# Optimization experiments

Measured on AMD Instinct MI355X. Metric: run time of the kernel, lower is better.

Reference implementation:

```python
import jax, jax.numpy as jnp
import numpy as np

B, C, I, E, K, H, W = 8, 16, 1, 256, 3, 256, 256  # batch, channels, input_dim, embedding_dim, kernel, spatial
NUM_CH = 64  # embedding vocabulary (num_channels)
PAD = 1


def setup_inputs() -> dict:
    key = jax.random.key(0)
    k1, k2, k3 = jax.random.split(key, 3)
    x = jax.random.normal(k1, (B, C, I, H, W), dtype=jnp.float32)
    indices = jax.random.randint(k2, (B, C), 0, NUM_CH)
    emb_weight = jax.random.normal(k3, (NUM_CH, I * E * K * K), dtype=jnp.float32) * 0.05
    bias = jnp.zeros((1, E, 1, 1), dtype=jnp.float32)
    return {"x": x, "indices": indices, "emb_weight": emb_weight, "bias": bias}


def reference(x, indices, emb_weight, bias):
    # Gather per-(sample, channel) conv weights: [B, C, I*E*K*K]
    w = emb_weight[indices].astype(x.dtype)
    w = w.reshape(B, C, I, E, K, K)
    # Encoder conv path: permute(0,3,1,2,4,5) -> [B, E, C, I, K, K] -> [B*E, C*I, K, K]
    w = jnp.transpose(w, (0, 3, 1, 2, 4, 5)).reshape(B * E, C * I, K, K)
    # x -> [1, B*C*I, H, W]; grouped conv with groups=B
    xr = x.reshape(1, B * C * I, H, W)
    y = jax.lax.conv_general_dilated(
        xr, w,
        window_strides=(1, 1),
        padding=[(PAD, PAD), (PAD, PAD)],
        feature_group_count=B,
        dimension_numbers=("NCHW", "OIHW", "NCHW"),
    )
    y = y.reshape(B, E, H, W) + bias
    return y
```

## Files before the change

### kernel.cpp

```cpp
#include <hip/hip_runtime.h>
#include <hip/hip_bf16.h>

#define BB 8
#define CC 16
#define EE 256
#define HH 256
#define WW 256
#define EMB_ROW (EE*9)

typedef __attribute__((ext_vector_type(8)))  __bf16 bf16x8;
typedef __attribute__((ext_vector_type(16))) float  f32x16;
typedef __attribute__((ext_vector_type(4)))  float  f32x4;

#define LDS_X_OFF   9216
#define SLOT_BYTES  8256
#define LDS_EPI_OFF 42240
#define LDS_TOTAL   75008

#define NTASK 2064

__device__ __forceinline__ unsigned pack_bf2(float a, float b) {
    union { __hip_bfloat162 h; unsigned u; } t;
    t.h.x = __float2bfloat16(a);
    t.h.y = __float2bfloat16(b);
    return t.u;
}

__device__ __forceinline__ int xswz(int wp, int inner) {
    return ((wp << 5) | inner) ^ ((wp & 4) << 2);
}

__global__ __launch_bounds__(512, 4) void conv_fused(
    const float* __restrict__ x,
    const int*   __restrict__ indices,
    const float* __restrict__ emb,
    const float* __restrict__ bias,
    float*       __restrict__ out)
{
    __shared__ __align__(16) char smem[LDS_TOTAL];
    char*  WB  = smem;
    char*  XB  = smem + LDS_X_OFF;
    float* EPI = (float*)(smem + LDS_EPI_OFF);

    const int b  = blockIdx.x;
    const int hc = blockIdx.y;
    const int ez = blockIdx.z;
    const int tid   = threadIdx.x;
    const int lane  = tid & 63;
    const int wid   = tid >> 6;
    const int l31   = lane & 31;
    const int lhalf = lane >> 5;
    const int e0 = ez * 32;
    const int w0 = wid * 32;
    const int h0 = hc * 16;

    {
        const int e = tid >> 4, c = tid & 15;
        const int idx = indices[b * CC + c];
        const float* wrow = emb + (size_t)idx * EMB_ROW + (size_t)(e0 + e) * 9;
        #pragma unroll
        for (int tap = 0; tap < 9; ++tap) {
            *reinterpret_cast<__hip_bfloat16*>(WB + tap * 1024 + e * 32 + c * 2) =
                __float2bfloat16(wrow[tap]);
        }
    }

    float r0[5], r1[5];
    auto issue_loads = [&](int ir) {
        #pragma unroll
        for (int k = 0; k < 5; ++k) {
            const int u = tid + 512 * k;
            if (u < NTASK) {
                const int cp = u / 258;
                const int wp = u - cp * 258;
                const int iw = wp - 1;
                const bool v = ((unsigned)iw < 256u) && ((unsigned)ir < 256u);
                const float* p = x + (((size_t)(b * CC + 2 * cp) * HH + (ir & 255)) * WW + (iw & 255));
                r0[k] = v ? p[0] : 0.f;
                r1[k] = v ? p[HH * WW] : 0.f;
            }
        }
    };
    auto write_stage = [&](int ir) {
        const int slot = (ir + 1) & 3;
        #pragma unroll
        for (int k = 0; k < 5; ++k) {
            const int u = tid + 512 * k;
            if (u < NTASK) {
                const int cp = u / 258;
                const int wp = u - cp * 258;
                *reinterpret_cast<unsigned*>(XB + slot * SLOT_BYTES + xswz(wp, cp << 2)) =
                    pack_bf2(r0[k], r1[k]);
            }
        }
    };

    issue_loads(h0 - 1); write_stage(h0 - 1);
    issue_loads(h0);     write_stage(h0);
    issue_loads(h0 + 1); write_stage(h0 + 1);
    issue_loads(h0 + 2);
    asm volatile("s_waitcnt lgkmcnt(0)" ::: "memory");
    __builtin_amdgcn_s_barrier();

    bf16x8 afrag[9];
    #pragma unroll
    for (int tap = 0; tap < 9; ++tap)
        afrag[tap] = *reinterpret_cast<const bf16x8*>(WB + tap * 1024 + l31 * 32 + lhalf * 16);

    float bb[4];
    #pragma unroll
    for (int i = 0; i < 4; ++i) bb[i] = bias[e0 + wid * 4 + i];

    for (int h = h0; h < h0 + 16; ++h) {
        if (h + 2 <= h0 + 16) write_stage(h + 2);
        if (h + 3 <= h0 + 16) issue_loads(h + 3);
        asm volatile("s_waitcnt lgkmcnt(0)" ::: "memory");
        __builtin_amdgcn_s_barrier();

        f32x16 acc;
        #pragma unroll
        for (int r = 0; r < 16; ++r) acc[r] = 0.f;

        #pragma unroll
        for (int kh = 0; kh < 3; ++kh) {
            const char* base = XB + ((h + kh) & 3) * SLOT_BYTES;
            #pragma unroll
            for (int kw = 0; kw < 3; ++kw) {
                const int wp = w0 + l31 + kw;
                bf16x8 bfrag = *reinterpret_cast<const bf16x8*>(base + xswz(wp, lhalf << 4));
                acc = __builtin_amdgcn_mfma_f32_32x32x16_bf16(afrag[kh * 3 + kw], bfrag, acc, 0, 0, 0);
            }
        }

        #pragma unroll
        for (int r = 0; r < 16; ++r) {
            const int erow = (r & 3) + 8 * (r >> 2) + 4 * lhalf;
            EPI[erow * 256 + w0 + l31] = acc[r];
        }
        asm volatile("s_waitcnt lgkmcnt(0)" ::: "memory");
        __builtin_amdgcn_s_barrier();

        #pragma unroll
        for (int i = 0; i < 4; ++i) {
            const int e = wid * 4 + i;
            f32x4 v = *reinterpret_cast<const f32x4*>(&EPI[e * 256 + lane * 4]);
            v += bb[i];
            __builtin_nontemporal_store(v,
                reinterpret_cast<f32x4*>(&out[((size_t)(b * EE + e0 + e) * HH + h) * WW + lane * 4]));
        }
    }
}

extern "C" void kernel_launch(void* const* d_in, const int* in_sizes, int n_in,
                              void* d_out, int out_size, void* d_ws, size_t ws_size,
                              hipStream_t stream) {
    const float* x       = (const float*)d_in[0];
    const int*   indices = (const int*)  d_in[1];
    const float* emb     = (const float*)d_in[2];
    const float* bias    = (const float*)d_in[3];
    float*       out     = (float*)d_out;

    conv_fused<<<dim3(BB, 16, 8), dim3(512), 0, stream>>>(x, indices, emb, bias, out);
}
```

Before: 111.9 us.

## Split epilogue staging into halves to shrink LDS and raise occupancy

Result: slower. 345.9 us (+209.1%).

```diff
diff --git a/kernel.cpp b/kernel.cpp
--- a/kernel.cpp
+++ b/kernel.cpp
@@ -12,10 +12,10 @@
 typedef __attribute__((ext_vector_type(16))) float  f32x16;
 typedef __attribute__((ext_vector_type(4)))  float  f32x4;
 
-#define LDS_X_OFF   9216
+#define LDS_EPI_OFF 0
+#define LDS_X_OFF   16384
 #define SLOT_BYTES  8256
-#define LDS_EPI_OFF 42240
-#define LDS_TOTAL   75008
+#define LDS_TOTAL   (16384 + 4*8256)
 
 #define NTASK 2064
 
@@ -30,7 +30,10 @@
     return ((wp << 5) | inner) ^ ((wp & 4) << 2);
 }
 
-__global__ __launch_bounds__(512, 4) void conv_fused(
+#define BARRIER() do { asm volatile("s_waitcnt lgkmcnt(0)" ::: "memory"); \
+                       __builtin_amdgcn_s_barrier(); } while (0)
+
+__global__ __launch_bounds__(512, 6) void conv_fused(
     const float* __restrict__ x,
     const int*   __restrict__ indices,
     const float* __restrict__ emb,
@@ -39,8 +42,8 @@
 {
     __shared__ __align__(16) char smem[LDS_TOTAL];
     char*  WB  = smem;
+    float* EPI = (float*)(smem + LDS_EPI_OFF);
     char*  XB  = smem + LDS_X_OFF;
-    float* EPI = (float*)(smem + LDS_EPI_OFF);
 
     const int b  = blockIdx.x;
     const int hc = blockIdx.y;
@@ -99,23 +102,24 @@
     issue_loads(h0);     write_stage(h0);
     issue_loads(h0 + 1); write_stage(h0 + 1);
     issue_loads(h0 + 2);
-    asm volatile("s_waitcnt lgkmcnt(0)" ::: "memory");
-    __builtin_amdgcn_s_barrier();
+    BARRIER();
 
     bf16x8 afrag[9];
     #pragma unroll
     for (int tap = 0; tap < 9; ++tap)
         afrag[tap] = *reinterpret_cast<const bf16x8*>(WB + tap * 1024 + l31 * 32 + lhalf * 16);
 
-    float bb[4];
+    float bb0[2], bb1[2];
     #pragma unroll
-    for (int i = 0; i < 4; ++i) bb[i] = bias[e0 + wid * 4 + i];
+    for (int i = 0; i < 2; ++i) {
+        bb0[i] = bias[e0 + 2 * wid + i];
+        bb1[i] = bias[e0 + 16 + 2 * wid + i];
+    }
 
     for (int h = h0; h < h0 + 16; ++h) {
         if (h + 2 <= h0 + 16) write_stage(h + 2);
         if (h + 3 <= h0 + 16) issue_loads(h + 3);
-        asm volatile("s_waitcnt lgkmcnt(0)" ::: "memory");
-        __builtin_amdgcn_s_barrier();
+        BARRIER();
 
         f32x16 acc;
         #pragma unroll
@@ -133,20 +137,34 @@
         }
 
         #pragma unroll
-        for (int r = 0; r < 16; ++r) {
+        for (int r = 0; r < 8; ++r) {
             const int erow = (r & 3) + 8 * (r >> 2) + 4 * lhalf;
             EPI[erow * 256 + w0 + l31] = acc[r];
         }
-        asm volatile("s_waitcnt lgkmcnt(0)" ::: "memory");
-        __builtin_amdgcn_s_barrier();
+        BARRIER();
+        #pragma unroll
+        for (int i = 0; i < 2; ++i) {
+            const int row = 2 * wid + i;
+            f32x4 v = *reinterpret_cast<const f32x4*>(&EPI[row * 256 + lane * 4]);
+            v += bb0[i];
+            __builtin_nontemporal_store(v,
+                reinterpret_cast<f32x4*>(&out[((size_t)(b * EE + e0 + row) * HH + h) * WW + lane * 4]));
+        }
+        BARRIER();
 
         #pragma unroll
-        for (int i = 0; i < 4; ++i) {
-            const int e = wid * 4 + i;
-            f32x4 v = *reinterpret_cast<const f32x4*>(&EPI[e * 256 + lane * 4]);
-            v += bb[i];
+        for (int r = 8; r < 16; ++r) {
+            const int erow = (r & 3) + 8 * (r >> 2) + 4 * lhalf - 16;
+            EPI[erow * 256 + w0 + l31] = acc[r];
+        }
+        BARRIER();
+        #pragma unroll
+        for (int i = 0; i < 2; ++i) {
+            const int row = 2 * wid + i;
+            f32x4 v = *reinterpret_cast<const f32x4*>(&EPI[row * 256 + lane * 4]);
+            v += bb1[i];
             __builtin_nontemporal_store(v,
-                reinterpret_cast<f32x4*>(&out[((size_t)(b * EE + e0 + e) * HH + h) * WW + lane * 4]));
+                reinterpret_cast<f32x4*>(&out[((size_t)(b * EE + e0 + 16 + row) * HH + h) * WW + lane * 4]));
         }
     }
 }
```
